# Kernel tuning notes

Hardware: AMD Instinct MI355X
Metric: run time of the kernel (lower is better)

The kernel has to match this reference:

```python
import jax, jax.numpy as jnp
import numpy as np

T = 1024          # num tokens
H = 2048          # hidden_size
NH = 16           # attention heads
NKV = 4           # kv heads (GQA)
HD = 128          # head_dim
E = 32            # num routed experts
K = 4             # top_k
I = 1024          # moe_intermediate_size
NS = 1            # num_shared_experts
EPS = 1e-6
THETA = 600000.0  # rope base
SCALE = HD ** -0.5


def rmsnorm(x, w):
    return x * jax.lax.rsqrt(jnp.mean(x * x, axis=-1, keepdims=True) + EPS) * w


def rope(x, positions):
    # x: [T, n_heads, HD], neox-style rotation on full head_dim
    half = HD // 2
    inv_freq = 1.0 / (THETA ** (jnp.arange(half, dtype=jnp.float32) / half))
    ang = positions.astype(jnp.float32)[:, None] * inv_freq        # [T, half]
    cos = jnp.cos(ang)[:, None, :]
    sin = jnp.sin(ang)[:, None, :]
    x1, x2 = x[..., :half], x[..., half:]
    return jnp.concatenate([x1 * cos - x2 * sin, x1 * sin + x2 * cos], axis=-1)


def setup_inputs() -> dict:
    key = jax.random.key(0)
    ks = jax.random.split(key, 10)
    s = 0.02
    return {
        "hidden_states": jax.random.normal(ks[0], (T, H), dtype=jnp.float32),
        "positions": jnp.arange(T, dtype=jnp.int32),
        "w_rms1": jnp.ones((H,), jnp.float32),
        "w_rms2": jnp.ones((H,), jnp.float32),
        "w_qkv": jax.random.normal(ks[1], ((NH + 2 * NKV) * HD, H), jnp.float32) * s,
        "w_o": jax.random.normal(ks[2], (H, NH * HD), jnp.float32) * s,
        "w_router": jax.random.normal(ks[3], (E, H), jnp.float32) * s,
        "w1": jax.random.normal(ks[4], (E, H, I), jnp.float32) * s,   # expert gate proj
        "w3": jax.random.normal(ks[5], (E, H, I), jnp.float32) * s,   # expert up proj
        "w2": jax.random.normal(ks[6], (E, I, H), jnp.float32) * s,   # expert down proj
        "ws_gate_up": jax.random.normal(ks[7], (2 * I * NS, H), jnp.float32) * s,
        "ws_down": jax.random.normal(ks[8], (H, I * NS), jnp.float32) * s,
    }


def reference(hidden_states, positions, w_rms1, w_rms2, w_qkv, w_o, w_router,
              w1, w3, w2, ws_gate_up, ws_down):
    x = hidden_states
    # ---- attention block ----
    h = rmsnorm(x, w_rms1)
    qkv = h @ w_qkv.T                                   # [T, (NH+2NKV)*HD]
    q = qkv[:, : NH * HD].reshape(T, NH, HD)
    k = qkv[:, NH * HD : (NH + NKV) * HD].reshape(T, NKV, HD)
    v = qkv[:, (NH + NKV) * HD :].reshape(T, NKV, HD)
    q = rope(q, positions)
    k = rope(k, positions)
    rep = NH // NKV
    k = jnp.repeat(k, rep, axis=1)                      # [T, NH, HD]
    v = jnp.repeat(v, rep, axis=1)
    scores = jnp.einsum("thd,shd->hts", q, k) * SCALE   # [NH, T, T]
    causal = jnp.tril(jnp.ones((T, T), dtype=bool))
    scores = jnp.where(causal, scores, -jnp.inf)
    attn = jax.nn.softmax(scores, axis=-1)
    o = jnp.einsum("hts,shd->thd", attn, v).reshape(T, NH * HD)
    x = x + o @ w_o.T                                   # residual
    # ---- MoE block ----
    h2 = rmsnorm(x, w_rms2)
    # router in fp32 (router_dtype default)
    logits = h2.astype(jnp.float32) @ w_router.T        # [T, E]
    probs = jax.nn.softmax(logits, axis=-1)
    topv, topi = jax.lax.top_k(probs, K)                # [T, K]
    topv = topv / jnp.sum(topv, axis=-1, keepdims=True)  # norm_topk_prob
    combine = jnp.zeros((T, E), jnp.float32).at[jnp.arange(T)[:, None], topi].add(topv)
    combine = combine.astype(h2.dtype)                  # routed_scaling_factor = 1.0
    g = jnp.einsum("th,ehi->tei", h2, w1)               # [T, E, I]
    u = jnp.einsum("th,ehi->tei", h2, w3)
    a = jax.nn.silu(g) * u                              # SiluAndMul
    d = jnp.einsum("tei,eih->teh", a, w2)               # [T, E, H]
    routed = jnp.einsum("teh,te->th", d, combine)
    # shared expert MLP
    gu = h2 @ ws_gate_up.T                              # [T, 2*I*NS]
    gs, us = gu[:, : I * NS], gu[:, I * NS :]
    shared = (jax.nn.silu(gs) * us) @ ws_down.T
    return x + routed + shared
```

## Files before the change

### kernel.cpp

```cpp
#include <hip/hip_runtime.h>
#include <hip/hip_bf16.h>
#include <math.h>
#include <stdint.h>

#define T_ 1024
#define H_ 2048
#define NH_ 16
#define NKV_ 4
#define HD_ 128
#define E_ 32
#define TOPK_ 4
#define I_ 1024
#define QKVN_ 3072
#define EPS_ 1e-6f
#define THETA_ 600000.0f
#define SCALE_ 0.08838834764831845f

typedef unsigned short u16;
typedef u16 u16x4 __attribute__((ext_vector_type(4)));
typedef u16 u16x8 __attribute__((ext_vector_type(8)));
typedef __bf16 bf16x8 __attribute__((ext_vector_type(8)));
typedef float f32x4 __attribute__((ext_vector_type(4)));

__device__ __forceinline__ u16 f2b(float f) {
  unsigned u = __builtin_bit_cast(unsigned, f);
  u += 0x7FFFu + ((u >> 16) & 1u);
  return (u16)(u >> 16);
}
__device__ __forceinline__ float b2f(u16 x) {
  unsigned u = ((unsigned)x) << 16;
  return __builtin_bit_cast(float, u);
}
__device__ __forceinline__ int swz8(int r) { return ((r ^ (r >> 3)) & 7) << 3; }

__device__ __forceinline__ void gload16(const void* g, void* l) {
  __builtin_amdgcn_global_load_lds(
      reinterpret_cast<const __attribute__((address_space(1))) unsigned int*>(
          reinterpret_cast<uintptr_t>(g)),
      reinterpret_cast<__attribute__((address_space(3))) unsigned int*>(
          reinterpret_cast<uintptr_t>(l)),
      16, 0, 0);
}

template<int EPI, bool GATHER>
__global__ __launch_bounds__(512, 6) void moe_gemm_k(
    const u16* __restrict__ A, const float* __restrict__ B, const float* __restrict__ B2,
    float* __restrict__ O1, float* __restrict__ O2,
    int NW, int lda, int ldb, int kchunk,
    const int* __restrict__ eoff, const int* __restrict__ slots,
    const float* __restrict__ slotw, long long sBz)
{
  __shared__ u16 As[2][64 * 32];
  __shared__ float Bsf[2][32 * 128];

  const int e = blockIdx.y >> 3;
  const int mb = blockIdx.y & 7;
  const int goff = eoff[e];
  const int Mloc = eoff[e + 1] - goff;
  const int m0 = mb * 64;
  if (m0 >= Mloc) return;

  const int xx = blockIdx.x;
  const float* Bp;
  float* Op;
  int n0;
  if constexpr (EPI == 0) {
    int wsel = xx >> 3;
    n0 = (xx & 7) * 128;
    Bp = (wsel ? B2 : B) + (long long)e * sBz;
    Op = wsel ? O2 : O1;
  } else {
    n0 = xx * 128;
    Bp = B + (long long)e * sBz;
    Op = O1;
  }
  const int k0base = blockIdx.z * kchunk;
  const u16* Ae = GATHER ? A : (A + (long long)goff * lda);

  const int tid = threadIdx.x;
  const int lane = tid & 63;
  const int wv = tid >> 6;
  const int wm = wv >> 2, wn = wv & 3;
  const int hl = lane >> 5;

  const u16* Abase = nullptr;
  if (wv < 4) {
    int r = wv * 16 + (lane >> 2);
    int rr = m0 + r;
    if (rr > Mloc - 1) rr = Mloc - 1;
    long long grow = GATHER ? (long long)slots[goff + rr] : (long long)rr;
    Abase = Ae + grow * (long long)lda + (((lane & 3) ^ (r & 3)) << 3);
  }
  const int bcol = (4 * (lane & 31)) ^ ((wv >= 4) ? 16 : 0);

  f32x4 acc[2][2];
  #pragma unroll
  for (int m = 0; m < 2; ++m)
    #pragma unroll
    for (int n = 0; n < 2; ++n)
      acc[m][n] = f32x4{0.f, 0.f, 0.f, 0.f};

  auto stage = [&](int bf, int k0) {
    if (wv < 4) gload16(Abase + k0, &As[bf][wv * 512]);
    #pragma unroll
    for (int p = 0; p < 2; ++p) {
      int row = p * 16 + wv * 2 + hl;
      const float* src = Bp + (long long)(k0 + row) * ldb + n0 + bcol;
      gload16(src, &Bsf[bf][(p * 16 + wv * 2) * 128]);
    }
  };

  const int kg = lane >> 4;
  const int cr = lane & 15;

  stage(0, k0base);
  __syncthreads();

  int buf = 0;
  for (int ks = 0; ks < kchunk; ks += 32) {
    bool more = (ks + 32) < kchunk;
    if (more) stage(buf ^ 1, k0base + ks + 32);
    const u16* Ap = &As[buf][0];
    const float* Bq = &Bsf[buf][0];
    bf16x8 af[2];
    #pragma unroll
    for (int m = 0; m < 2; ++m) {
      int r = wm * 32 + m * 16 + cr;
      af[m] = __builtin_bit_cast(bf16x8,
          *(const u16x8*)(Ap + r * 32 + ((kg ^ (r & 3)) << 3)));
    }
    #pragma unroll
    for (int n = 0; n < 2; ++n) {
      int nfs = (wn * 32 + n * 16 + cr) ^ ((kg & 1) << 4);
      u16x8 bb;
      #pragma unroll
      for (int j = 0; j < 8; ++j) bb[j] = f2b(Bq[(kg * 8 + j) * 128 + nfs]);
      bf16x8 bfr = __builtin_bit_cast(bf16x8, bb);
      #pragma unroll
      for (int m = 0; m < 2; ++m)
        acc[m][n] = __builtin_amdgcn_mfma_f32_16x16x32_bf16(af[m], bfr, acc[m][n], 0, 0, 0);
    }
    __syncthreads();
    buf ^= 1;
  }

  const int rq = lane >> 4;
  #pragma unroll
  for (int m = 0; m < 2; ++m) {
    #pragma unroll
    for (int j = 0; j < 4; ++j) {
      int row = m0 + wm * 32 + m * 16 + rq * 4 + j;
      if (row >= Mloc) continue;
      if constexpr (EPI == 0) {
        float* dst = Op + (long long)(goff + row) * NW;
        #pragma unroll
        for (int n = 0; n < 2; ++n) {
          int col = n0 + wn * 32 + n * 16 + cr;
          atomicAdd(dst + col, acc[m][n][j]);
        }
      } else {
        int tok = slots[goff + row];
        float wgt = slotw[goff + row];
        float* dst = Op + (long long)tok * NW;
        #pragma unroll
        for (int n = 0; n < 2; ++n) {
          int col = n0 + wn * 32 + n * 16 + cr;
          atomicAdd(dst + col, wgt * acc[m][n][j]);
        }
      }
    }
  }
}

template<typename TB, bool BTL, bool GROUPED, bool GATHER, int EPI>
__global__ __launch_bounds__(256) void gemm_k(
    const u16* __restrict__ A, const TB* __restrict__ B, const TB* __restrict__ B2,
    u16* __restrict__ Cb, u16* __restrict__ Cb2, float* __restrict__ Cf,
    const float* __restrict__ res1, const float* __restrict__ res2,
    int M, int N, int K, int lda, int ldb, int ldc,
    float alpha, int causal, int mbmax, int yhalf,
    const int* __restrict__ eoff, const int* __restrict__ slots,
    const float* __restrict__ slotw,
    long long sAz, long long sBz, long long sCz, int bdivz)
{
  __shared__ u16 As[2][8192];
  __shared__ u16 Bs[2][8192];

  int m0, n0, Mloc, goff = 0;
  const u16* Ae = A;
  const TB* Be = B;
  u16* Cw = Cb;
  if (GROUPED) {
    int e = blockIdx.x / mbmax;
    int mb = blockIdx.x - e * mbmax;
    goff = eoff[e];
    Mloc = eoff[e + 1] - goff;
    m0 = mb * 128;
    if (m0 >= Mloc) return;
    int by = blockIdx.y;
    if (yhalf && by >= yhalf) {
      n0 = (by - yhalf) * 128;
      Be = B2 + (long long)e * sBz;
      Cw = Cb2;
    } else {
      n0 = by * 128;
      Be = B + (long long)e * sBz;
    }
    if (!GATHER) Ae = A + (long long)goff * lda;
  } else {
    m0 = blockIdx.x * 128;
    n0 = blockIdx.y * 128;
    Mloc = M;
    long long z = blockIdx.z;
    Ae = A + z * sAz;
    Be = B + (long long)(z / bdivz) * sBz;
    if (Cb) Cw = Cb + z * sCz;
    if (causal == 1 && n0 > m0 + 127) return;
  }

  const int tid = threadIdx.x;
  const int lane = tid & 63;
  const int wv = tid >> 6;
  const int wr = wv >> 1, wc = wv & 1;

  int kend = K;
  if (causal == 2) { int ke = m0 + 128; if (ke < kend) kend = ke; }

  f32x4 acc[4][4];
  #pragma unroll
  for (int i = 0; i < 4; ++i)
    #pragma unroll
    for (int j = 0; j < 4; ++j)
      acc[i][j] = f32x4{0.f, 0.f, 0.f, 0.f};

  auto stageA = [&](int bf, int k0) {
    #pragma unroll
    for (int it = 0; it < 4; ++it) {
      int r = it * 32 + (tid >> 3);
      int kk = (tid & 7) * 8;
      int rr = m0 + r;
      if (rr > Mloc - 1) rr = Mloc - 1;
      long long row = GATHER ? (long long)slots[goff + rr] : (long long)rr;
      const u16* src = Ae + row * (long long)lda + k0 + (kk ^ swz8(r));
      gload16(src, &As[bf][it * 2048 + (tid & ~63) * 8]);
    }
  };

  float4 bregT[8];
  float brKN[32];
  u16x8 bvKN[4];

  auto loadB = [&](int bf, int k0) {
    if constexpr (BTL) {
      if constexpr (sizeof(TB) == 4) {
        const float* Bf = (const float*)Be;
        #pragma unroll
        for (int it = 0; it < 8; ++it) {
          int idx = it * 1024 + tid * 4;
          int n = idx >> 6, kk = idx & 63;
          bregT[it] = *(const float4*)(Bf + (long long)(n0 + n) * ldb + k0 + kk);
        }
      } else {
        const u16* Bb = (const u16*)Be;
        #pragma unroll
        for (int it = 0; it < 4; ++it) {
          int r = it * 32 + (tid >> 3);
          int kk = (tid & 7) * 8;
          const u16* src = Bb + (long long)(n0 + r) * ldb + k0 + (kk ^ swz8(r));
          gload16(src, &Bs[bf][it * 2048 + (tid & ~63) * 8]);
        }
      }
    } else {
      if constexpr (sizeof(TB) == 4) {
        const float* Bf = (const float*)Be;
        int n = (tid & 63) + ((tid >> 7) << 6);
        int ks = ((tid >> 6) & 1) * 32;
        const float* bp = Bf + (long long)(k0 + ks) * ldb + n0 + n;
        #pragma unroll
        for (int j = 0; j < 32; ++j) brKN[j] = bp[(long long)j * ldb];
      } else {
        const u16* Bb = (const u16*)Be;
        int nb = (tid & 15) * 8;
        int ks = (tid >> 4) * 4;
        #pragma unroll
        for (int i = 0; i < 4; ++i)
          bvKN[i] = *(const u16x8*)(Bb + (long long)(k0 + ks + i) * ldb + n0 + nb);
      }
    }
  };

  auto writeB = [&](int bf) {
    if constexpr (BTL) {
      if constexpr (sizeof(TB) == 4) {
        #pragma unroll
        for (int it = 0; it < 8; ++it) {
          int idx = it * 1024 + tid * 4;
          int n = idx >> 6, kk = idx & 63;
          float4 f = bregT[it];
          u16x4 o = u16x4{f2b(f.x), f2b(f.y), f2b(f.z), f2b(f.w)};
          *(u16x4*)(&Bs[bf][n * 64 + (kk ^ swz8(n))]) = o;
        }
      }
    } else {
      if constexpr (sizeof(TB) == 4) {
        int n = (tid & 63) + ((tid >> 7) << 6);
        int ks = ((tid >> 6) & 1) * 32;
        #pragma unroll
        for (int p = 0; p < 4; ++p) {
          u16x8 o;
          #pragma unroll
          for (int q = 0; q < 8; ++q) o[q] = f2b(brKN[p * 8 + q]);
          *(u16x8*)(&Bs[bf][n * 64 + ((ks + p * 8) ^ swz8(n))]) = o;
        }
      } else {
        int nb = (tid & 15) * 8;
        int ks = (tid >> 4) * 4;
        #pragma unroll
        for (int q = 0; q < 8; ++q) {
          int n = nb + q;
          u16x4 o = u16x4{bvKN[0][q], bvKN[1][q], bvKN[2][q], bvKN[3][q]};
          *(u16x4*)(&Bs[bf][n * 64 + (ks ^ swz8(n))]) = o;
        }
      }
    }
  };

  const int ar = (wr << 6) + (lane & 15);
  const int bc = (wc << 6) + (lane & 15);
  int aoff[4], asw[4], boff[4], bsw[4];
  #pragma unroll
  for (int m = 0; m < 4; ++m) {
    int r = ar + m * 16; aoff[m] = r * 64; asw[m] = swz8(r);
    int rb = bc + m * 16; boff[m] = rb * 64; bsw[m] = swz8(rb);
  }

  stageA(0, 0);
  loadB(0, 0);
  writeB(0);
  __syncthreads();

  int buf = 0;
  for (int k0 = 0; k0 < kend; k0 += 64) {
    int nk = k0 + 64;
    bool more = nk < kend;
    if (more) { stageA(buf ^ 1, nk); loadB(buf ^ 1, nk); }
    const u16* Ap = &As[buf][0];
    const u16* Bp = &Bs[buf][0];
    #pragma unroll
    for (int kk = 0; kk < 64; kk += 32) {
      int kb = kk + ((lane >> 4) << 3);
      bf16x8 af[4], bfr[4];
      #pragma unroll
      for (int m = 0; m < 4; ++m)
        af[m] = __builtin_bit_cast(bf16x8, *(const u16x8*)(Ap + aoff[m] + (kb ^ asw[m])));
      #pragma unroll
      for (int n = 0; n < 4; ++n)
        bfr[n] = __builtin_bit_cast(bf16x8, *(const u16x8*)(Bp + boff[n] + (kb ^ bsw[n])));
      #pragma unroll
      for (int m = 0; m < 4; ++m)
        #pragma unroll
        for (int n = 0; n < 4; ++n)
          acc[m][n] = __builtin_amdgcn_mfma_f32_16x16x32_bf16(af[m], bfr[n], acc[m][n], 0, 0, 0);
    }
    if (more) writeB(buf ^ 1);
    __syncthreads();
    buf ^= 1;
  }

  const int cr = lane & 15, rq = lane >> 4;
  #pragma unroll
  for (int m = 0; m < 4; ++m) {
    #pragma unroll
    for (int j = 0; j < 4; ++j) {
      int row = m0 + (wr << 6) + m * 16 + rq * 4 + j;
      if (row >= Mloc) continue;
      #pragma unroll
      for (int n = 0; n < 4; ++n) {
        int col = n0 + (wc << 6) + n * 16 + cr;
        float v = acc[m][n][j];
        long long o = (long long)(goff + row) * ldc + col;
        if constexpr (EPI == 0) {
          Cw[o] = f2b(v);
        } else if constexpr (EPI == 1) {
          Cw[o] = f2b(v * alpha);
        } else if constexpr (EPI == 2) {
          Cf[o] = res1[o] + v;
        } else if constexpr (EPI == 3) {
          int tok = slots[goff + row];
          float wgt = slotw[goff + row];
          atomicAdd(&Cf[(long long)tok * ldc + col], wgt * v);
        } else {
          Cf[o] = res1[o] + res2[o] + v;
        }
      }
    }
  }
}

__global__ __launch_bounds__(256) void rmsnorm_k(const float* __restrict__ x,
                                                 const float* __restrict__ w,
                                                 u16* __restrict__ outb,
                                                 float* __restrict__ outf) {
  int t = blockIdx.x;
  int tid = threadIdx.x;
  const float* xr = x + (long long)t * H_;
  float4 a = *(const float4*)(xr + tid * 8);
  float4 b = *(const float4*)(xr + tid * 8 + 4);
  float ss = a.x * a.x + a.y * a.y + a.z * a.z + a.w * a.w +
             b.x * b.x + b.y * b.y + b.z * b.z + b.w * b.w;
  #pragma unroll
  for (int o = 32; o; o >>= 1) ss += __shfl_down(ss, o);
  __shared__ float red[4];
  if ((tid & 63) == 0) red[tid >> 6] = ss;
  __syncthreads();
  float sc = rsqrtf((red[0] + red[1] + red[2] + red[3]) * (1.0f / H_) + EPS_);
  float vo[8] = {a.x, a.y, a.z, a.w, b.x, b.y, b.z, b.w};
  const float* wr = w + tid * 8;
  u16x8 ob;
  #pragma unroll
  for (int q = 0; q < 8; ++q) {
    float val = vo[q] * sc * wr[q];
    ob[q] = f2b(val);
    if (outf) outf[(long long)t * H_ + tid * 8 + q] = val;
  }
  *(u16x8*)(outb + (long long)t * H_ + tid * 8) = ob;
}

__global__ __launch_bounds__(256) void rope_k(const u16* __restrict__ qkv,
                                              const int* __restrict__ pos,
                                              u16* __restrict__ q_r,
                                              u16* __restrict__ k_r,
                                              u16* __restrict__ v_r) {
  int t = blockIdx.x;
  int tid = threadIdx.x;
  float p = (float)pos[t];
  const u16* row = qkv + (long long)t * QKVN_;
  const float cfac = logf(THETA_) * (1.0f / 64.0f);
  #pragma unroll
  for (int it = 0; it < 4; ++it) {
    int item = it * 256 + tid;
    int h = item >> 6, d = item & 63;
    float inv = expf(-cfac * (float)d);
    float ang = p * inv;
    float c = cosf(ang), s = sinf(ang);
    float x1v = b2f(row[h * 128 + d]);
    float x2v = b2f(row[h * 128 + 64 + d]);
    u16* dst = q_r + ((long long)h * T_ + t) * HD_;
    dst[d] = f2b(x1v * c - x2v * s);
    dst[d + 64] = f2b(x1v * s + x2v * c);
  }
  {
    int item = tid;
    int kv = item >> 6, d = item & 63;
    float inv = expf(-cfac * (float)d);
    float ang = p * inv;
    float c = cosf(ang), s = sinf(ang);
    float x1v = b2f(row[NH_ * HD_ + kv * 128 + d]);
    float x2v = b2f(row[NH_ * HD_ + kv * 128 + 64 + d]);
    u16* dst = k_r + ((long long)kv * T_ + t) * HD_;
    dst[d] = f2b(x1v * c - x2v * s);
    dst[d + 64] = f2b(x1v * s + x2v * c);
  }
  #pragma unroll
  for (int it = 0; it < 2; ++it) {
    int item = it * 256 + tid;
    int kv = item >> 7, d = item & 127;
    v_r[((long long)kv * T_ + t) * HD_ + d] = row[(NH_ + NKV_) * HD_ + kv * 128 + d];
  }
}

__global__ __launch_bounds__(64) void softmax_k(u16* __restrict__ P) {
  int r = blockIdx.x;
  int h = r >> 10, i = r & 1023;
  u16* row = P + ((long long)h * T_ + i) * T_;
  int lane = threadIdx.x;
  int n = i + 1;
  float vals[16];
  float mx = -1e30f;
  #pragma unroll
  for (int it = 0; it < 16; ++it) {
    int j = it * 64 + lane;
    float s = (j < n) ? b2f(row[j]) : -1e30f;
    vals[it] = s;
    mx = fmaxf(mx, s);
  }
  #pragma unroll
  for (int o = 32; o; o >>= 1) mx = fmaxf(mx, __shfl_xor(mx, o));
  float sum = 0.f;
  #pragma unroll
  for (int it = 0; it < 16; ++it) {
    int j = it * 64 + lane;
    float e = (j < n) ? __expf(vals[it] - mx) : 0.f;
    vals[it] = e;
    sum += e;
  }
  #pragma unroll
  for (int o = 32; o; o >>= 1) sum += __shfl_xor(sum, o);
  float inv = 1.f / sum;
  #pragma unroll
  for (int it = 0; it < 16; ++it) {
    int j = it * 64 + lane;
    row[j] = f2b(vals[it] * inv);
  }
}

__global__ __launch_bounds__(64) void router_k(const float* __restrict__ h2,
                                               const float* __restrict__ wr,
                                               float* __restrict__ logits) {
  int b = blockIdx.x;
  int t = b >> 5, e = b & 31;
  const float* xr = h2 + (long long)t * H_;
  const float* wv = wr + (long long)e * H_;
  int lane = threadIdx.x;
  float s = 0.f;
  #pragma unroll
  for (int it = 0; it < 8; ++it) {
    int h = it * 256 + lane * 4;
    float4 a = *(const float4*)(xr + h);
    float4 w4 = *(const float4*)(wv + h);
    s += a.x * w4.x + a.y * w4.y + a.z * w4.z + a.w * w4.w;
  }
  #pragma unroll
  for (int o = 32; o; o >>= 1) s += __shfl_xor(s, o);
  if (lane == 0) logits[b] = s;
}

__global__ __launch_bounds__(256) void topk_k(const float* __restrict__ logits,
                                              int* __restrict__ topi,
                                              float* __restrict__ topw) {
  int t = blockIdx.x * 256 + threadIdx.x;
  if (t >= T_) return;
  float l[E_];
  #pragma unroll
  for (int e = 0; e < E_; ++e) l[e] = logits[t * E_ + e];
  int sel[TOPK_];
  float sv[TOPK_];
  unsigned used = 0;
  for (int j = 0; j < TOPK_; ++j) {
    float best = -1e30f;
    int bi = 0;
    for (int e = 0; e < E_; ++e) {
      if (used & (1u << e)) continue;
      if (l[e] > best) { best = l[e]; bi = e; }
    }
    used |= 1u << bi;
    sel[j] = bi;
    sv[j] = best;
  }
  float mx = sv[0];
  float s = 0.f;
  #pragma unroll
  for (int j = 0; j < TOPK_; ++j) { sv[j] = __expf(sv[j] - mx); s += sv[j]; }
  float inv = 1.f / s;
  #pragma unroll
  for (int j = 0; j < TOPK_; ++j) {
    topi[t * TOPK_ + j] = sel[j];
    topw[t * TOPK_ + j] = sv[j] * inv;
  }
}

__global__ __launch_bounds__(256) void hist_k(const int* __restrict__ topi, int* __restrict__ cnt) {
  int idx = blockIdx.x * 256 + threadIdx.x;
  if (idx < T_ * TOPK_) atomicAdd(&cnt[topi[idx]], 1);
}

__global__ __launch_bounds__(64) void scan_k(const int* __restrict__ cnt,
                                             int* __restrict__ eoff,
                                             int* __restrict__ cursor) {
  if (threadIdx.x == 0) {
    int s = 0;
    for (int e = 0; e < E_; ++e) { eoff[e] = s; cursor[e] = s; s += cnt[e]; }
    eoff[E_] = s;
  }
}

__global__ __launch_bounds__(256) void scatter_k(const int* __restrict__ topi,
                                                 const float* __restrict__ topw,
                                                 int* __restrict__ cursor,
                                                 int* __restrict__ slots,
                                                 float* __restrict__ slotw) {
  int idx = blockIdx.x * 256 + threadIdx.x;
  if (idx >= T_ * TOPK_) return;
  int e = topi[idx];
  int pos = atomicAdd(&cursor[e], 1);
  slots[pos] = idx >> 2;
  slotw[pos] = topw[idx];
}

__global__ __launch_bounds__(256) void silumul_f_k(const float* __restrict__ g,
                                                   const float* __restrict__ u,
                                                   u16* __restrict__ a) {
  long long idx = ((long long)blockIdx.x * 256 + threadIdx.x) * 8;
  float4 g0 = *(const float4*)(g + idx);
  float4 g1 = *(const float4*)(g + idx + 4);
  float4 u0 = *(const float4*)(u + idx);
  float4 u1 = *(const float4*)(u + idx + 4);
  float gv[8] = {g0.x, g0.y, g0.z, g0.w, g1.x, g1.y, g1.z, g1.w};
  float uv[8] = {u0.x, u0.y, u0.z, u0.w, u1.x, u1.y, u1.z, u1.w};
  u16x8 o;
  #pragma unroll
  for (int q = 0; q < 8; ++q) {
    float x = gv[q];
    float sl = x / (1.f + __expf(-x));
    o[q] = f2b(sl * uv[q]);
  }
  *(u16x8*)(a + idx) = o;
}

__global__ __launch_bounds__(256) void sharedact_k(const u16* __restrict__ gu,
                                                   u16* __restrict__ act) {
  long long idx = ((long long)blockIdx.x * 256 + threadIdx.x) * 8;
  long long t = idx >> 10;
  int i = (int)(idx & 1023);
  const u16* row = gu + t * (2 * I_);
  u16x8 g = *(const u16x8*)(row + i);
  u16x8 u = *(const u16x8*)(row + I_ + i);
  u16x8 o;
  #pragma unroll
  for (int q = 0; q < 8; ++q) {
    float x = b2f(g[q]);
    float y = b2f(u[q]);
    float sl = x / (1.f + __expf(-x));
    o[q] = f2b(sl * y);
  }
  *(u16x8*)(act + t * I_ + i) = o;
}

extern "C" void kernel_launch(void* const* d_in, const int* in_sizes, int n_in,
                              void* d_out, int out_size, void* d_ws, size_t ws_size,
                              hipStream_t stream) {
  const float* x        = (const float*)d_in[0];
  const int* positions  = (const int*)d_in[1];
  const float* w_rms1   = (const float*)d_in[2];
  const float* w_rms2   = (const float*)d_in[3];
  const float* w_qkv    = (const float*)d_in[4];
  const float* w_o      = (const float*)d_in[5];
  const float* w_router = (const float*)d_in[6];
  const float* w1       = (const float*)d_in[7];
  const float* w3       = (const float*)d_in[8];
  const float* w2       = (const float*)d_in[9];
  const float* ws_gu    = (const float*)d_in[10];
  const float* ws_dn    = (const float*)d_in[11];
  float* out = (float*)d_out;

  char* ws = (char*)d_ws;
  size_t off = 0;
  auto alloc = [&](size_t bytes) {
    size_t o = off;
    off = (off + bytes + 255) & ~(size_t)255;
    return (void*)(ws + o);
  };
  u16*  h1b     = (u16*)alloc((size_t)T_ * H_ * 2);
  u16*  qkvb    = (u16*)alloc((size_t)T_ * QKVN_ * 2);
  u16*  q_r     = (u16*)alloc((size_t)NH_ * T_ * HD_ * 2);
  u16*  k_r     = (u16*)alloc((size_t)NKV_ * T_ * HD_ * 2);
  u16*  v_r     = (u16*)alloc((size_t)NKV_ * T_ * HD_ * 2);
  u16*  scoresP = (u16*)alloc((size_t)NH_ * T_ * T_ * 2);
  u16*  o_attn  = (u16*)alloc((size_t)T_ * H_ * 2);
  float* x1     = (float*)alloc((size_t)T_ * H_ * 4);
  float* h2f    = (float*)alloc((size_t)T_ * H_ * 4);
  u16*  h2b     = (u16*)alloc((size_t)T_ * H_ * 2);
  u16*  gub     = (u16*)alloc((size_t)T_ * 2 * I_ * 2);
  u16*  actsh   = (u16*)alloc((size_t)T_ * I_ * 2);
  float* logits = (float*)alloc((size_t)T_ * E_ * 4);
  int*  topi    = (int*)alloc((size_t)T_ * TOPK_ * 4);
  float* topw   = (float*)alloc((size_t)T_ * TOPK_ * 4);
  int*  cnt     = (int*)alloc(E_ * 4);
  int*  eoffp   = (int*)alloc((E_ + 1) * 4);
  int*  cursor  = (int*)alloc(E_ * 4);
  int*  slots   = (int*)alloc((size_t)T_ * TOPK_ * 4);
  float* slotw  = (float*)alloc((size_t)T_ * TOPK_ * 4);
  u16*  a_g     = (u16*)alloc((size_t)T_ * TOPK_ * I_ * 2);
  float* routed = (float*)alloc((size_t)T_ * H_ * 4);

  float* g_f32 = (float*)scoresP;
  float* u_f32 = g_f32 + (size_t)T_ * TOPK_ * I_;

  hipMemsetAsync(routed, 0, (size_t)T_ * H_ * 4, stream);
  hipMemsetAsync(cnt, 0, E_ * 4, stream);

  rmsnorm_k<<<T_, 256, 0, stream>>>(x, w_rms1, h1b, nullptr);

  gemm_k<float, true, false, false, 0><<<dim3(8, 24, 1), 256, 0, stream>>>(
      h1b, w_qkv, nullptr, qkvb, nullptr, nullptr, nullptr, nullptr,
      T_, QKVN_, H_, H_, H_, QKVN_, 1.f, 0, 1, 0, nullptr, nullptr, nullptr, 0, 0, 0, 1);

  rope_k<<<T_, 256, 0, stream>>>(qkvb, positions, q_r, k_r, v_r);

  gemm_k<u16, true, false, false, 1><<<dim3(8, 8, NH_), 256, 0, stream>>>(
      q_r, k_r, nullptr, scoresP, nullptr, nullptr, nullptr, nullptr,
      T_, T_, HD_, HD_, HD_, T_, SCALE_, 1, 1, 0, nullptr, nullptr, nullptr,
      (long long)T_ * HD_, (long long)T_ * HD_, (long long)T_ * T_, NH_ / NKV_);

  softmax_k<<<NH_ * T_, 64, 0, stream>>>(scoresP);

  gemm_k<u16, false, false, false, 0><<<dim3(8, 1, NH_), 256, 0, stream>>>(
      scoresP, v_r, nullptr, o_attn, nullptr, nullptr, nullptr, nullptr,
      T_, HD_, T_, T_, HD_, H_, 1.f, 2, 1, 0, nullptr, nullptr, nullptr,
      (long long)T_ * T_, (long long)T_ * HD_, (long long)HD_, NH_ / NKV_);

  gemm_k<float, true, false, false, 2><<<dim3(8, 16, 1), 256, 0, stream>>>(
      o_attn, w_o, nullptr, nullptr, nullptr, x1, x, nullptr,
      T_, H_, H_, H_, H_, H_, 1.f, 0, 1, 0, nullptr, nullptr, nullptr, 0, 0, 0, 1);

  hipMemsetAsync(g_f32, 0, (size_t)T_ * TOPK_ * I_ * 8, stream);

  rmsnorm_k<<<T_, 256, 0, stream>>>(x1, w_rms2, h2b, h2f);

  router_k<<<T_ * E_, 64, 0, stream>>>(h2f, w_router, logits);
  topk_k<<<4, 256, 0, stream>>>(logits, topi, topw);
  hist_k<<<16, 256, 0, stream>>>(topi, cnt);
  scan_k<<<1, 64, 0, stream>>>(cnt, eoffp, cursor);
  scatter_k<<<16, 256, 0, stream>>>(topi, topw, cursor, slots, slotw);

  moe_gemm_k<0, true><<<dim3(16, E_ * 8, 4), 512, 0, stream>>>(
      h2b, w1, w3, g_f32, u_f32,
      I_, H_, I_, H_ / 4, eoffp, slots, nullptr, (long long)H_ * I_);
  silumul_f_k<<<(T_ * TOPK_ * I_) / (256 * 8), 256, 0, stream>>>(g_f32, u_f32, a_g);

  moe_gemm_k<1, false><<<dim3(16, E_ * 8, 4), 512, 0, stream>>>(
      a_g, w2, nullptr, routed, nullptr,
      H_, I_, H_, I_ / 4, eoffp, slots, slotw, (long long)I_ * H_);

  gemm_k<float, true, false, false, 0><<<dim3(8, 16, 1), 256, 0, stream>>>(
      h2b, ws_gu, nullptr, gub, nullptr, nullptr, nullptr, nullptr,
      T_, 2 * I_, H_, H_, H_, 2 * I_, 1.f, 0, 1, 0, nullptr, nullptr, nullptr, 0, 0, 0, 1);
  sharedact_k<<<(T_ * I_) / (256 * 8), 256, 0, stream>>>(gub, actsh);

  gemm_k<float, true, false, false, 4><<<dim3(8, 16, 1), 256, 0, stream>>>(
      actsh, ws_dn, nullptr, nullptr, nullptr, out, x1, routed,
      T_, H_, I_, I_, I_, H_, 1.f, 0, 1, 0, nullptr, nullptr, nullptr, 0, 0, 0, 1);
}
```

Before: 639.0 us.

## Convert MoE expert weights to bf16 on staging into transposed LDS tiles

The MoE GEMM now loads fp32 expert-weight tiles into registers, converts them to bf16 once, and writes them into a swizzled, k-contiguous bf16 LDS layout. Before, raw fp32 tiles were staged in LDS and converted element by element before every MFMA. MFMA B operands become single vector LDS reads, and LDS use per buffer is halved. The split-K factor drops from 4 to 2, halving atomic partial-sum traffic, and launch bounds raise the occupancy target. The catch is that B loads now go through registers instead of direct-to-LDS, which costs register pressure and gives less parallelism per expert.

```diff
diff --git a/kernel.cpp b/kernel.cpp
--- a/kernel.cpp
+++ b/kernel.cpp
@@ -43,7 +43,7 @@
 }
 
 template<int EPI, bool GATHER>
-__global__ __launch_bounds__(512, 6) void moe_gemm_k(
+__global__ __launch_bounds__(512, 8) void moe_gemm_k(
     const u16* __restrict__ A, const float* __restrict__ B, const float* __restrict__ B2,
     float* __restrict__ O1, float* __restrict__ O2,
     int NW, int lda, int ldb, int kchunk,
@@ -51,7 +51,7 @@
     const float* __restrict__ slotw, long long sBz)
 {
   __shared__ u16 As[2][64 * 32];
-  __shared__ float Bsf[2][32 * 128];
+  __shared__ u16 Bs[2][128 * 32];
 
   const int e = blockIdx.y >> 3;
   const int mb = blockIdx.y & 7;
@@ -81,7 +81,6 @@
   const int lane = tid & 63;
   const int wv = tid >> 6;
   const int wm = wv >> 2, wn = wv & 3;
-  const int hl = lane >> 5;
 
   const u16* Abase = nullptr;
   if (wv < 4) {
@@ -91,7 +90,27 @@
     long long grow = GATHER ? (long long)slots[goff + rr] : (long long)rr;
     Abase = Ae + grow * (long long)lda + (((lane & 3) ^ (r & 3)) << 3);
   }
-  const int bcol = (4 * (lane & 31)) ^ ((wv >= 4) ? 16 : 0);
+
+  const int bn = tid & 127;
+  const int bkb = (tid >> 7) << 3;
+  const float* Bbase = Bp + (long long)bkb * ldb + n0 + bn;
+  const int bws = bn * 32 + (bkb ^ ((((bn ^ (bn >> 3)) & 3)) << 3));
+
+  float br[8];
+  auto loadB = [&](int k0) {
+    const float* p = Bbase + (long long)k0 * ldb;
+    #pragma unroll
+    for (int j = 0; j < 8; ++j) br[j] = p[(long long)j * ldb];
+  };
+  auto writeB = [&](int bf) {
+    u16x8 o;
+    #pragma unroll
+    for (int j = 0; j < 8; ++j) o[j] = f2b(br[j]);
+    *(u16x8*)(&Bs[bf][bws]) = o;
+  };
+  auto stageA = [&](int bf, int k0) {
+    if (wv < 4) gload16(Abase + k0, &As[bf][wv * 512]);
+  };
 
   f32x4 acc[2][2];
   #pragma unroll
@@ -100,46 +119,45 @@
     for (int n = 0; n < 2; ++n)
       acc[m][n] = f32x4{0.f, 0.f, 0.f, 0.f};
 
-  auto stage = [&](int bf, int k0) {
-    if (wv < 4) gload16(Abase + k0, &As[bf][wv * 512]);
-    #pragma unroll
-    for (int p = 0; p < 2; ++p) {
-      int row = p * 16 + wv * 2 + hl;
-      const float* src = Bp + (long long)(k0 + row) * ldb + n0 + bcol;
-      gload16(src, &Bsf[bf][(p * 16 + wv * 2) * 128]);
-    }
-  };
-
   const int kg = lane >> 4;
   const int cr = lane & 15;
 
-  stage(0, k0base);
+  int aoff[2], boff[2];
+  #pragma unroll
+  for (int m = 0; m < 2; ++m) {
+    int r = wm * 32 + m * 16 + cr;
+    aoff[m] = r * 32 + ((kg ^ (r & 3)) << 3);
+  }
+  #pragma unroll
+  for (int n = 0; n < 2; ++n) {
+    int c = wn * 32 + n * 16 + cr;
+    boff[n] = c * 32 + ((kg ^ ((c ^ (c >> 3)) & 3)) << 3);
+  }
+
+  loadB(k0base);
+  stageA(0, k0base);
+  writeB(0);
   __syncthreads();
 
   int buf = 0;
   for (int ks = 0; ks < kchunk; ks += 32) {
     bool more = (ks + 32) < kchunk;
-    if (more) stage(buf ^ 1, k0base + ks + 32);
+    if (more) { loadB(k0base + ks + 32); stageA(buf ^ 1, k0base + ks + 32); }
     const u16* Ap = &As[buf][0];
-    const float* Bq = &Bsf[buf][0];
-    bf16x8 af[2];
-    #pragma unroll
-    for (int m = 0; m < 2; ++m) {
-      int r = wm * 32 + m * 16 + cr;
-      af[m] = __builtin_bit_cast(bf16x8,
-          *(const u16x8*)(Ap + r * 32 + ((kg ^ (r & 3)) << 3)));
-    }
-    #pragma unroll
-    for (int n = 0; n < 2; ++n) {
-      int nfs = (wn * 32 + n * 16 + cr) ^ ((kg & 1) << 4);
-      u16x8 bb;
+    const u16* Bq = &Bs[buf][0];
+    bf16x8 af[2], bfr[2];
+    #pragma unroll
+    for (int m = 0; m < 2; ++m)
+      af[m] = __builtin_bit_cast(bf16x8, *(const u16x8*)(Ap + aoff[m]));
+    #pragma unroll
+    for (int n = 0; n < 2; ++n)
+      bfr[n] = __builtin_bit_cast(bf16x8, *(const u16x8*)(Bq + boff[n]));
+    #pragma unroll
+    for (int m = 0; m < 2; ++m)
       #pragma unroll
-      for (int j = 0; j < 8; ++j) bb[j] = f2b(Bq[(kg * 8 + j) * 128 + nfs]);
-      bf16x8 bfr = __builtin_bit_cast(bf16x8, bb);
-      #pragma unroll
-      for (int m = 0; m < 2; ++m)
-        acc[m][n] = __builtin_amdgcn_mfma_f32_16x16x32_bf16(af[m], bfr, acc[m][n], 0, 0, 0);
-    }
+      for (int n = 0; n < 2; ++n)
+        acc[m][n] = __builtin_amdgcn_mfma_f32_16x16x32_bf16(af[m], bfr[n], acc[m][n], 0, 0, 0);
+    if (more) writeB(buf ^ 1);
     __syncthreads();
     buf ^= 1;
   }
@@ -713,14 +731,14 @@
   scan_k<<<1, 64, 0, stream>>>(cnt, eoffp, cursor);
   scatter_k<<<16, 256, 0, stream>>>(topi, topw, cursor, slots, slotw);
 
-  moe_gemm_k<0, true><<<dim3(16, E_ * 8, 4), 512, 0, stream>>>(
+  moe_gemm_k<0, true><<<dim3(16, E_ * 8, 2), 512, 0, stream>>>(
       h2b, w1, w3, g_f32, u_f32,
-      I_, H_, I_, H_ / 4, eoffp, slots, nullptr, (long long)H_ * I_);
+      I_, H_, I_, H_ / 2, eoffp, slots, nullptr, (long long)H_ * I_);
   silumul_f_k<<<(T_ * TOPK_ * I_) / (256 * 8), 256, 0, stream>>>(g_f32, u_f32, a_g);
 
-  moe_gemm_k<1, false><<<dim3(16, E_ * 8, 4), 512, 0, stream>>>(
+  moe_gemm_k<1, false><<<dim3(16, E_ * 8, 2), 512, 0, stream>>>(
       a_g, w2, nullptr, routed, nullptr,
-      H_, I_, H_, I_ / 4, eoffp, slots, slotw, (long long)I_ * H_);
+      H_, I_, H_, I_ / 2, eoffp, slots, slotw, (long long)I_ * H_);
 
   gemm_k<float, true, false, false, 0><<<dim3(8, 16, 1), 256, 0, stream>>>(
       h2b, ws_gu, nullptr, gub, nullptr, nullptr, nullptr, nullptr,
```

Result: faster. 607.5 us (-4.9%).
